# Kernel tuning notes

Measured on AMD Instinct MI355X. Metric: run time of the kernel, lower is better.

Reference implementation:

```python
import jax, jax.numpy as jnp
import numpy as np

B, L, D, N = 4, 2048, 1024, 8
H = D // N  # head_dim = 128
EPS = 1e-6


def _ln(x, gamma, beta, axes):
    m = jnp.mean(x, axis=axes, keepdims=True)
    v = jnp.mean(jnp.square(x - m), axis=axes, keepdims=True)
    return (x - m) * jax.lax.rsqrt(v + EPS) * gamma + beta


def setup_inputs() -> dict:
    key = jax.random.key(0)
    ks = jax.random.split(key, 8)
    glorot_d = (6.0 / (D + D)) ** 0.5  # GlorotUniform over fan_in=D, fan_out=N*H=D
    inputs = jax.random.normal(ks[0], (B, L, D), dtype=jnp.float32)
    attention_mask = jnp.tril(jnp.ones((L, L), dtype=bool))[None].repeat(B, axis=0)
    return {
        'inputs': inputs,
        'attention_mask': attention_mask,
        'ln_in_gamma': jnp.ones((D,), jnp.float32),
        'ln_in_beta': jnp.zeros((D,), jnp.float32),
        'wu': jax.random.uniform(ks[1], (D, N, H), jnp.float32, -glorot_d, glorot_d),
        'wq': jax.random.uniform(ks[2], (D, N, H), jnp.float32, -glorot_d, glorot_d),
        'wk': jax.random.uniform(ks[3], (D, N, H), jnp.float32, -glorot_d, glorot_d),
        'wv': jax.random.uniform(ks[4], (D, N, H), jnp.float32, -glorot_d, glorot_d),
        'ln_attn_gamma': jnp.ones((N, H), jnp.float32),
        'ln_attn_beta': jnp.zeros((N, H), jnp.float32),
        'wo': jax.random.uniform(ks[5], (N, H, D), jnp.float32, -glorot_d, glorot_d),
    }


def reference(inputs, attention_mask, ln_in_gamma, ln_in_beta, wu, wq, wk, wv,
              ln_attn_gamma, ln_attn_beta, wo):
    x = _ln(inputs, ln_in_gamma, ln_in_beta, axes=-1)  # [B,L,D]
    u = jax.nn.silu(jnp.einsum('btd,dnh->btnh', x, wu))
    q = jax.nn.silu(jnp.einsum('btd,dnh->btnh', x, wq))
    k = jax.nn.silu(jnp.einsum('btd,dnh->btnh', x, wk))
    v = jax.nn.silu(jnp.einsum('btd,dnh->btnh', x, wv))
    # pointwise silu attention, normalized by sequence length
    qk = jnp.einsum('bthd,bshd->bhts', q, k)  # [B,N,L,L]
    seq_len = q.shape[1]
    attn = jax.nn.silu(qk) / seq_len
    attn = jnp.where(attention_mask[:, None, :, :], attn, 0.0)
    attn_out = jnp.einsum('bhts,bshd->bthd', attn, v)  # [B,L,N,H]
    normed = _ln(attn_out, ln_attn_gamma, ln_attn_beta, axes=(-2, -1))
    out = jnp.einsum('btnh,nhd->btd', u * normed, wo)
    return out + inputs
```

## Files before the change

### kernel.cpp

```cpp
#include <hip/hip_runtime.h>
#include <hip/hip_bf16.h>
#include <stdint.h>

#define D_    1024
#define L_    2048
#define B_    4
#define NHEAD 8
#define HDIM  128
#define BL_   (B_*L_)
#define EPS_  1e-6f

typedef __attribute__((ext_vector_type(8))) short short8;
typedef __attribute__((ext_vector_type(4))) float f32x4;

__device__ __forceinline__ unsigned short f2bf(float f) {
  unsigned u = __builtin_bit_cast(unsigned, f);
  unsigned r = 0x7fffu + ((u >> 16) & 1u);
  return (unsigned short)((u + r) >> 16);
}
__device__ __forceinline__ float bf2f(unsigned short h) {
  return __builtin_bit_cast(float, ((unsigned)h) << 16);
}
__device__ __forceinline__ float silu_f(float x) {
  return x * __builtin_amdgcn_rcpf(1.f + __expf(-x));
}
__device__ __forceinline__ unsigned cvt_pk_bf16(float lo, float hi) {
  unsigned r;
  asm("v_cvt_pk_bf16_f32 %0, %1, %2" : "=v"(r) : "v"(lo), "v"(hi));
  return r;
}

__device__ __forceinline__ void gll16(const void* g, void* l) {
  auto gp = reinterpret_cast<const __attribute__((address_space(1))) unsigned*>(
      reinterpret_cast<uintptr_t>(g));
  auto lp = reinterpret_cast<__attribute__((address_space(3))) unsigned*>(
      (unsigned)reinterpret_cast<uintptr_t>(l));
  __builtin_amdgcn_global_load_lds(gp, lp, 16, 0, 0);
}

__global__ __launch_bounds__(256) void wt_kernel(
    const float* __restrict__ wu, const float* __restrict__ wq,
    const float* __restrict__ wk, const float* __restrict__ wv,
    const float* __restrict__ wo, unsigned short* __restrict__ wt)
{
  __shared__ float t[64][65];
  int mat = blockIdx.z;
  const float* src = mat==0?wu: mat==1?wq: mat==2?wk: mat==3?wv: wo;
  unsigned short* dst = wt + (size_t)mat*D_*D_;
  int r0 = blockIdx.y*64, c0 = blockIdx.x*64;
  int tid = threadIdx.x;
  for (int i = 0; i < 16; ++i) {
    int e = i*256 + tid; int r = e>>6, c = e&63;
    t[r][c] = src[(size_t)(r0+r)*D_ + c0 + c];
  }
  __syncthreads();
  for (int i = 0; i < 16; ++i) {
    int e = i*256 + tid; int r = e>>6, c = e&63;
    dst[(size_t)(c0+r)*D_ + r0 + c] = f2bf(t[c][r]);
  }
}

__global__ __launch_bounds__(256) void ln_in_kernel(
    const float* __restrict__ in, const float* __restrict__ gamma,
    const float* __restrict__ beta, unsigned short* __restrict__ x)
{
  int row = blockIdx.x, tid = threadIdx.x;
  float4 v = ((const float4*)(in + (size_t)row*D_))[tid];
  float s = v.x+v.y+v.z+v.w;
  float ss = v.x*v.x + v.y*v.y + v.z*v.z + v.w*v.w;
  #pragma unroll
  for (int o = 32; o; o >>= 1) { s += __shfl_down(s,o); ss += __shfl_down(ss,o); }
  __shared__ float red[8];
  int lane = tid&63, wid = tid>>6;
  if (lane==0) { red[wid]=s; red[4+wid]=ss; }
  __syncthreads();
  s = red[0]+red[1]+red[2]+red[3];
  ss = red[4]+red[5]+red[6]+red[7];
  float mean = s * (1.f/D_);
  float var  = ss * (1.f/D_) - mean*mean;
  float rstd = rsqrtf(var + EPS_);
  float4 g = ((const float4*)gamma)[tid], b = ((const float4*)beta)[tid];
  ushort4 o;
  o.x = f2bf((v.x-mean)*rstd*g.x + b.x);
  o.y = f2bf((v.y-mean)*rstd*g.y + b.y);
  o.z = f2bf((v.z-mean)*rstd*g.z + b.z);
  o.w = f2bf((v.w-mean)*rstd*g.w + b.w);
  ((ushort4*)(x + (size_t)row*D_))[tid] = o;
}

template<int MODE>
__global__ __launch_bounds__(512) __attribute__((amdgpu_waves_per_eu(2,2))) void gemm8p(
    const unsigned short* __restrict__ A, const unsigned short* __restrict__ Bt,
    unsigned short* __restrict__ o_u, unsigned short* __restrict__ o_q,
    unsigned short* __restrict__ o_k, unsigned short* __restrict__ o_vt,
    const float* __restrict__ resid, float* __restrict__ o_f)
{
  constexpr int BN  = (MODE==0) ? 256 : 128;
  constexpr int WN  = (MODE==0) ? 4 : 2;
  constexpr int WTM = (MODE==0) ? 128 : 64;
  constexpr int MF  = WTM/16;
  constexpr int BNS = BN*32;
  constexpr int BOFF = 32768;
  constexpr int RG  = BN/64;
  constexpr int NBCHW = (BNS/512)/8;
  const int K = 1024;

  __shared__ unsigned short lds[BOFF + 4*BNS];

  int lane = threadIdx.x & 63, wid = threadIdx.x >> 6;
  int wr = wid / WN, wc = wid % WN;
  int m0 = blockIdx.x * 256;
  int n0 = blockIdx.y * BN;
  const unsigned short* Ab = A + (size_t)m0*K;
  const unsigned short* Bb = Bt + (size_t)n0*K;

  f32x4 acc[MF][4] = {};

  auto stage = [&](int dbs, int k0) {
    #pragma unroll
    for (int j = 0; j < 2; ++j) {
      int c = wid*2 + j;
      int row = (c&3)*64 + lane;
      int kof = k0 + ((c>>2)<<3);
      gll16(Ab + (size_t)row*K + kof, &lds[dbs*8192 + c*512]);
    }
    #pragma unroll
    for (int j = 0; j < NBCHW; ++j) {
      int c = wid*NBCHW + j;
      int kk8 = c / RG, rg = c % RG;
      int row = rg*64 + lane;
      int kof = k0 + (kk8<<3);
      gll16(Bb + (size_t)row*K + kof, &lds[BOFF + dbs*BNS + c*512]);
    }
  };

  #pragma unroll
  for (int gp = 0; gp < 4; ++gp) stage(gp, gp*32);
  if constexpr (MODE==0) asm volatile("s_waitcnt vmcnt(12)" ::: "memory");
  else                   asm volatile("s_waitcnt vmcnt(9)"  ::: "memory");
  __builtin_amdgcn_s_barrier();

  auto do_phase = [&](int g, bool dostage) {
    const int bs = g & 3;
    const int kk4 = lane>>4, l15 = lane&15;
    short8 af[MF], bfr[4];
    const int ab = bs*8192 + kk4*2048 + (wr*WTM + l15)*8;
    #pragma unroll
    for (int m = 0; m < MF; ++m) af[m] = *(const short8*)&lds[ab + m*128];
    const int bb = BOFF + bs*BNS + kk4*(BN*8) + (wc*64 + l15)*8;
    #pragma unroll
    for (int n = 0; n < 4; ++n) bfr[n] = *(const short8*)&lds[bb + n*128];
    if (dostage) {
      int tp = g + 3;
      int k0 = (tp < 32 ? tp : 31) * 32;
      stage(tp & 3, k0);
    }
    __builtin_amdgcn_sched_barrier(0);
    __builtin_amdgcn_s_barrier();
    asm volatile("s_waitcnt lgkmcnt(0)" ::: "memory");
    __builtin_amdgcn_sched_barrier(0);
    __builtin_amdgcn_s_setprio(1);
    #pragma unroll
    for (int m = 0; m < MF; ++m)
      #pragma unroll
      for (int n = 0; n < 4; ++n)
        acc[m][n] = __builtin_amdgcn_mfma_f32_16x16x32_bf16(af[m], bfr[n], acc[m][n], 0,0,0);
    __builtin_amdgcn_s_setprio(0);
    if constexpr (MODE==0) asm volatile("s_waitcnt vmcnt(8)" ::: "memory");
    else                   asm volatile("s_waitcnt vmcnt(6)" ::: "memory");
    __builtin_amdgcn_sched_barrier(0);
    __builtin_amdgcn_s_barrier();
  };

  do_phase(0, false);
  #pragma unroll
  for (int g = 1; g < 32; ++g) do_phase(g, true);

  if constexpr (MODE == 0) {
    int mat = n0 >> 10;
    int jb = n0 & 1023;
    #pragma unroll
    for (int m = 0; m < MF; ++m) {
      int t_ = m0 + wr*WTM + m*16 + ((lane>>4)<<2);
      #pragma unroll
      for (int n = 0; n < 4; ++n) {
        int jj = jb + wc*64 + n*16 + (lane&15);
        float p0 = silu_f(acc[m][n][0]);
        float p1 = silu_f(acc[m][n][1]);
        float p2 = silu_f(acc[m][n][2]);
        float p3 = silu_f(acc[m][n][3]);
        if (mat == 3) {
          int b = t_ >> 11, tt = t_ & 2047;
          int nn = jj >> 7, h = jj & 127;
          ushort4 pk;
          pk.x = f2bf(p0); pk.y = f2bf(p1); pk.z = f2bf(p2); pk.w = f2bf(p3);
          *(ushort4*)&o_vt[(((size_t)(b*NHEAD+nn))*HDIM + h)*L_ + tt] = pk;
        } else {
          unsigned short* dst = mat==0 ? o_u : (mat==1 ? o_q : o_k);
          dst[(size_t)(t_+0)*D_ + jj] = f2bf(p0);
          dst[(size_t)(t_+1)*D_ + jj] = f2bf(p1);
          dst[(size_t)(t_+2)*D_ + jj] = f2bf(p2);
          dst[(size_t)(t_+3)*D_ + jj] = f2bf(p3);
        }
      }
    }
  } else {
    #pragma unroll
    for (int m = 0; m < MF; ++m) {
      int t_ = m0 + wr*WTM + m*16 + ((lane>>4)<<2);
      #pragma unroll
      for (int n = 0; n < 4; ++n) {
        int jj = n0 + wc*64 + n*16 + (lane&15);
        #pragma unroll
        for (int r = 0; r < 4; ++r)
          o_f[(size_t)(t_+r)*D_ + jj] = acc[m][n][r] + resid[(size_t)(t_+r)*D_ + jj];
      }
    }
  }
}

__global__ __launch_bounds__(512) __attribute__((amdgpu_waves_per_eu(2,2))) void attn_kernel(
    const unsigned short* __restrict__ gq, const unsigned short* __restrict__ gk,
    const unsigned short* __restrict__ gvt, unsigned short* __restrict__ attn_out)
{
  __shared__ unsigned short KP[16384];
  __shared__ unsigned short VT[16384];
  __shared__ unsigned short PA[16384];
  __shared__ unsigned short PB[16384];
  int id = blockIdx.x;
  int x = id & 7, c2 = (id >> 3) & 3, p = id >> 5;
  int bh = 8*c2 + x;
  int b = bh >> 3, n = bh & 7;
  int tiA = p, tiB = 15 - p;
  const unsigned short* qb = gq + (size_t)b*L_*D_ + n*HDIM;
  const unsigned short* kb = gk + (size_t)b*L_*D_ + n*HDIM;
  const unsigned short* vb = gvt + (size_t)bh*HDIM*L_;
  unsigned short* ob = attn_out + (size_t)b*L_*D_ + n*HDIM;
  int lane = threadIdx.x & 63, wid = threadIdx.x >> 6;
  int wsel = wid >> 2, wq = wid & 3;
  int wr = wq >> 1, wc = wq & 1;
  int hi = lane >> 4, l15 = lane & 15;
  int ti = wsel ? tiB : tiA;
  int t0 = ti * 128;
  unsigned short* Pbuf = wsel ? PB : PA;

  #pragma unroll
  for (int i = 0; i < 8; ++i) {
    int cc = wq*8 + i;
    int row = ((cc&1)<<6) + lane;
    int kof = (cc>>1)<<3;
    gll16(qb + (size_t)(t0+row)*D_ + kof, &Pbuf[cc*512]);
  }
  __syncthreads();
  short8 qf[4][4];
  #pragma unroll
  for (int kk = 0; kk < 4; ++kk) {
    int kbase = (kk*4 + hi)*1024;
    #pragma unroll
    for (int fn = 0; fn < 4; ++fn)
      qf[kk][fn] = *(const short8*)&Pbuf[kbase + (wc*64 + fn*16 + l15)*8];
  }
  __syncthreads();
  #pragma unroll
  for (int i = 0; i < 4; ++i) {
    int cc = wid*4 + i;
    int row = ((cc&1)<<6) + lane;
    int kof = (cc>>1)<<3;
    gll16(kb + (size_t)row*D_ + kof, &KP[cc*512]);
    gll16(vb + (size_t)row*L_ + kof, &VT[cc*512]);
  }
  __syncthreads();

  f32x4 oacc[4][4] = {};
  for (int st = 0; st <= tiB; ++st) {
    bool act = wsel ? true : (st <= tiA);
    bool stg = (st < tiB);
    f32x4 sacc[4][4] = {};
    if (act) {
      __builtin_amdgcn_s_setprio(1);
      #pragma unroll
      for (int kk = 0; kk < 4; ++kk) {
        int kbase = (kk*4 + hi)*1024;
        short8 kf[4];
        #pragma unroll
        for (int fm = 0; fm < 4; ++fm)
          kf[fm] = *(const short8*)&KP[kbase + (wr*64 + fm*16 + l15)*8];
        #pragma unroll
        for (int fm = 0; fm < 4; ++fm)
          #pragma unroll
          for (int fn = 0; fn < 4; ++fn)
            sacc[fm][fn] = __builtin_amdgcn_mfma_f32_16x16x32_bf16(kf[fm], qf[kk][fn], sacc[fm][fn], 0,0,0);
      }
      __builtin_amdgcn_s_setprio(0);
    }
    uint4 kreg[4];
    if (stg) {
      #pragma unroll
      for (int i = 0; i < 4; ++i) {
        int cc = wid*4 + i;
        int row = ((cc&1)<<6) + lane;
        int kof = (cc>>1)<<3;
        kreg[i] = *(const uint4*)(kb + (size_t)((st+1)*128 + row)*D_ + kof);
      }
    }
    if (act) {
      bool diag = (st == ti);
      #pragma unroll
      for (int fm = 0; fm < 4; ++fm) {
        int sb = wr*64 + fm*16 + (hi<<2);
        #pragma unroll
        for (int fn = 0; fn < 4; ++fn) {
          int tl = wc*64 + fn*16 + l15;
          float pv[4];
          #pragma unroll
          for (int r = 0; r < 4; ++r) {
            float sv = silu_f(sacc[fm][fn][r]) * (1.f/2048.f);
            if (diag && (tl < sb + r)) sv = 0.f;
            pv[r] = sv;
          }
          int a0 = (sb>>3)*1024 + tl*8 + (sb&7);
          *(unsigned*)&Pbuf[a0]   = cvt_pk_bf16(pv[0], pv[1]);
          *(unsigned*)&Pbuf[a0+2] = cvt_pk_bf16(pv[2], pv[3]);
        }
      }
    }
    asm volatile("s_waitcnt vmcnt(0) lgkmcnt(0)" ::: "memory");
    __builtin_amdgcn_sched_barrier(0);
    __builtin_amdgcn_s_barrier();
    __builtin_amdgcn_sched_barrier(0);
    if (stg) {
      #pragma unroll
      for (int i = 0; i < 4; ++i) {
        int cc = wid*4 + i;
        *(uint4*)&KP[cc*512 + (lane<<3)] = kreg[i];
      }
    }
    if (act) {
      __builtin_amdgcn_s_setprio(1);
      #pragma unroll
      for (int kk = 0; kk < 4; ++kk) {
        int kbase = (kk*4 + hi)*1024;
        short8 pa[4], vf[4];
        #pragma unroll
        for (int fm = 0; fm < 4; ++fm)
          pa[fm] = *(const short8*)&Pbuf[kbase + (wr*64 + fm*16 + l15)*8];
        #pragma unroll
        for (int fn = 0; fn < 4; ++fn)
          vf[fn] = *(const short8*)&VT[kbase + (wc*64 + fn*16 + l15)*8];
        #pragma unroll
        for (int fm = 0; fm < 4; ++fm)
          #pragma unroll
          for (int fn = 0; fn < 4; ++fn)
            oacc[fm][fn] = __builtin_amdgcn_mfma_f32_16x16x32_bf16(pa[fm], vf[fn], oacc[fm][fn], 0,0,0);
      }
      __builtin_amdgcn_s_setprio(0);
    }
    asm volatile("s_waitcnt lgkmcnt(0)" ::: "memory");
    __builtin_amdgcn_sched_barrier(0);
    __builtin_amdgcn_s_barrier();
    __builtin_amdgcn_sched_barrier(0);
    if (stg) {
      #pragma unroll
      for (int i = 0; i < 4; ++i) {
        int cc = wid*4 + i;
        int row = ((cc&1)<<6) + lane;
        int kof = (cc>>1)<<3;
        gll16(vb + (size_t)row*L_ + (st+1)*128 + kof, &VT[cc*512]);
      }
      __builtin_amdgcn_sched_barrier(0);
    }
  }
  #pragma unroll
  for (int fm = 0; fm < 4; ++fm) {
    int tl = wr*64 + fm*16 + (hi<<2);
    #pragma unroll
    for (int fn = 0; fn < 4; ++fn) {
      int h = wc*64 + fn*16 + l15;
      #pragma unroll
      for (int r = 0; r < 4; ++r)
        ob[(size_t)(t0 + tl + r)*D_ + h] = f2bf(oacc[fm][fn][r]);
    }
  }
}

__global__ __launch_bounds__(256) void ln_mul_kernel(
    const unsigned short* __restrict__ ain, const float* __restrict__ gamma,
    const float* __restrict__ beta, const unsigned short* __restrict__ u,
    unsigned short* __restrict__ y)
{
  int row = blockIdx.x, tid = threadIdx.x;
  ushort4 av = ((const ushort4*)(ain + (size_t)row*D_))[tid];
  float v0 = bf2f(av.x), v1 = bf2f(av.y), v2 = bf2f(av.z), v3 = bf2f(av.w);
  float s = v0+v1+v2+v3;
  float ss = v0*v0+v1*v1+v2*v2+v3*v3;
  #pragma unroll
  for (int o = 32; o; o >>= 1) { s += __shfl_down(s,o); ss += __shfl_down(ss,o); }
  __shared__ float red[8];
  int lane = tid&63, wid = tid>>6;
  if (lane==0) { red[wid]=s; red[4+wid]=ss; }
  __syncthreads();
  s = red[0]+red[1]+red[2]+red[3];
  ss = red[4]+red[5]+red[6]+red[7];
  float mean = s * (1.f/D_);
  float var  = ss * (1.f/D_) - mean*mean;
  float rstd = rsqrtf(var + EPS_);
  float4 g = ((const float4*)gamma)[tid], b = ((const float4*)beta)[tid];
  ushort4 uu = ((const ushort4*)(u + (size_t)row*D_))[tid];
  ushort4 o;
  o.x = f2bf(bf2f(uu.x) * ((v0-mean)*rstd*g.x + b.x));
  o.y = f2bf(bf2f(uu.y) * ((v1-mean)*rstd*g.y + b.y));
  o.z = f2bf(bf2f(uu.z) * ((v2-mean)*rstd*g.z + b.z));
  o.w = f2bf(bf2f(uu.w) * ((v3-mean)*rstd*g.w + b.w));
  ((ushort4*)(y + (size_t)row*D_))[tid] = o;
}

extern "C" void kernel_launch(void* const* d_in, const int* in_sizes, int n_in,
                              void* d_out, int out_size, void* d_ws, size_t ws_size,
                              hipStream_t stream) {
  const float* inputs = (const float*)d_in[0];
  const float* g_in = (const float*)d_in[2];
  const float* b_in = (const float*)d_in[3];
  const float* wu = (const float*)d_in[4];
  const float* wq = (const float*)d_in[5];
  const float* wk = (const float*)d_in[6];
  const float* wv = (const float*)d_in[7];
  const float* g_at = (const float*)d_in[8];
  const float* b_at = (const float*)d_in[9];
  const float* wo = (const float*)d_in[10];
  float* out = (float*)d_out;

  char* ws = (char*)d_ws;
  unsigned short* x   = (unsigned short*)(ws + ((size_t)0));
  unsigned short* q   = (unsigned short*)(ws + ((size_t)16<<20));
  unsigned short* k   = (unsigned short*)(ws + ((size_t)32<<20));
  unsigned short* u   = (unsigned short*)(ws + ((size_t)48<<20));
  unsigned short* vt  = (unsigned short*)(ws + ((size_t)64<<20));
  unsigned short* wt  = (unsigned short*)(ws + ((size_t)80<<20));
  unsigned short* ao  = (unsigned short*)(ws + ((size_t)96<<20));
  unsigned short* y = x;

  wt_kernel<<<dim3(16,16,5), 256, 0, stream>>>(wu, wq, wk, wv, wo, wt);
  ln_in_kernel<<<BL_, 256, 0, stream>>>(inputs, g_in, b_in, x);
  gemm8p<0><<<dim3(32,16), 512, 0, stream>>>(x, wt, u, q, k, vt, nullptr, nullptr);
  attn_kernel<<<256, 512, 0, stream>>>(q, k, vt, ao);
  ln_mul_kernel<<<BL_, 256, 0, stream>>>(ao, g_at, b_at, u, y);
  gemm8p<1><<<dim3(32,8), 512, 0, stream>>>(y, wt + (size_t)4*D_*D_,
                                            nullptr, nullptr, nullptr, nullptr, inputs, out);
}
```

Measured before the change: 279.9 us.

## Split attention KV range across wave groups and reduce partial outputs in LDS

Before, the two 4-wave groups of a block each handled a different query tile, paired p and 15-p, so the short-tile group sat idle for many steps. Now both groups work on the same query tile, and each takes half of every 128-key step (64 keys). The two query tiles are processed one after the other, and the partial outputs are summed through LDS before the store. This removes idle waves under the causal imbalance, at the cost of running both tiles in sequence, extra barriers, and an LDS reduction per tile.

New measurement: 257.0 us. 1.09x faster.

```diff
diff --git a/kernel.cpp b/kernel.cpp
--- a/kernel.cpp
+++ b/kernel.cpp
@@ -223,15 +223,11 @@
     const unsigned short* __restrict__ gq, const unsigned short* __restrict__ gk,
     const unsigned short* __restrict__ gvt, unsigned short* __restrict__ attn_out)
 {
-  __shared__ unsigned short KP[16384];
-  __shared__ unsigned short VT[16384];
-  __shared__ unsigned short PA[16384];
-  __shared__ unsigned short PB[16384];
+  __shared__ unsigned short SM[49152];
   int id = blockIdx.x;
-  int x = id & 7, c2 = (id >> 3) & 3, p = id >> 5;
+  int x = id & 7, c2 = (id >> 3) & 3, q = id >> 5;
   int bh = 8*c2 + x;
   int b = bh >> 3, n = bh & 7;
-  int tiA = p, tiB = 15 - p;
   const unsigned short* qb = gq + (size_t)b*L_*D_ + n*HDIM;
   const unsigned short* kb = gk + (size_t)b*L_*D_ + n*HDIM;
   const unsigned short* vb = gvt + (size_t)bh*HDIM*L_;
@@ -240,105 +236,102 @@
   int wsel = wid >> 2, wq = wid & 3;
   int wr = wq >> 1, wc = wq & 1;
   int hi = lane >> 4, l15 = lane & 15;
-  int ti = wsel ? tiB : tiA;
-  int t0 = ti * 128;
-  unsigned short* Pbuf = wsel ? PB : PA;
-
-  #pragma unroll
-  for (int i = 0; i < 8; ++i) {
-    int cc = wq*8 + i;
-    int row = ((cc&1)<<6) + lane;
-    int kof = (cc>>1)<<3;
-    gll16(qb + (size_t)(t0+row)*D_ + kof, &Pbuf[cc*512]);
-  }
-  __syncthreads();
-  short8 qf[4][4];
-  #pragma unroll
-  for (int kk = 0; kk < 4; ++kk) {
-    int kbase = (kk*4 + hi)*1024;
-    #pragma unroll
-    for (int fn = 0; fn < 4; ++fn)
-      qf[kk][fn] = *(const short8*)&Pbuf[kbase + (wc*64 + fn*16 + l15)*8];
-  }
-  __syncthreads();
-  #pragma unroll
-  for (int i = 0; i < 4; ++i) {
-    int cc = wid*4 + i;
-    int row = ((cc&1)<<6) + lane;
-    int kof = (cc>>1)<<3;
-    gll16(kb + (size_t)row*D_ + kof, &KP[cc*512]);
-    gll16(vb + (size_t)row*L_ + kof, &VT[cc*512]);
-  }
-  __syncthreads();
-
-  f32x4 oacc[4][4] = {};
-  for (int st = 0; st <= tiB; ++st) {
-    bool act = wsel ? true : (st <= tiA);
-    bool stg = (st < tiB);
-    f32x4 sacc[4][4] = {};
-    if (act) {
+  unsigned short* Kbuf = SM + (wsel ? 8192 : 0);
+  unsigned short* Vbuf = SM + 16384 + (wsel ? 8192 : 0);
+  unsigned short* Pbuf = SM + 32768 + (wsel ? 8192 : 0);
+  unsigned short* Qbuf = SM + 32768;
+  float* Cbuf = (float*)SM;
+
+  for (int uu = 0; uu < 2; ++uu) {
+    int ti = uu ? q : (15 - q);
+    int t0 = ti * 128;
+    #pragma unroll
+    for (int i = 0; i < 4; ++i) {
+      int cc = wid*4 + i;
+      gll16(qb + (size_t)(t0 + ((cc&1)<<6) + lane)*D_ + ((cc>>1)<<3), &Qbuf[cc*512]);
+    }
+    __syncthreads();
+    short8 qf[4][4];
+    #pragma unroll
+    for (int kk = 0; kk < 4; ++kk) {
+      int kbase = (kk*4 + hi)*1024;
+      #pragma unroll
+      for (int fn = 0; fn < 4; ++fn)
+        qf[kk][fn] = *(const short8*)&Qbuf[kbase + (wc*64 + fn*16 + l15)*8];
+    }
+    __syncthreads();
+    #pragma unroll
+    for (int i = 0; i < 4; ++i) {
+      int cc = wq*4 + i;
+      gll16(kb + (size_t)(wsel*64 + lane)*D_ + (cc<<3), &Kbuf[cc*512]);
+      gll16(vb + (size_t)(((cc&1)<<6) + lane)*L_ + wsel*64 + ((cc>>1)<<3), &Vbuf[cc*512]);
+    }
+    __syncthreads();
+
+    f32x4 oacc[4][4] = {};
+    for (int j = 0; j <= ti; ++j) {
+      bool stg = (j < ti);
+      int cnext = 2*(j+1) + wsel;
+      f32x4 sacc[2][4] = {};
       __builtin_amdgcn_s_setprio(1);
       #pragma unroll
       for (int kk = 0; kk < 4; ++kk) {
-        int kbase = (kk*4 + hi)*1024;
-        short8 kf[4];
-        #pragma unroll
-        for (int fm = 0; fm < 4; ++fm)
-          kf[fm] = *(const short8*)&KP[kbase + (wr*64 + fm*16 + l15)*8];
-        #pragma unroll
-        for (int fm = 0; fm < 4; ++fm)
+        int kbase = (kk*4 + hi)*512;
+        short8 kf[2];
+        #pragma unroll
+        for (int fm = 0; fm < 2; ++fm)
+          kf[fm] = *(const short8*)&Kbuf[kbase + (wr*32 + fm*16 + l15)*8];
+        #pragma unroll
+        for (int fm = 0; fm < 2; ++fm)
           #pragma unroll
           for (int fn = 0; fn < 4; ++fn)
             sacc[fm][fn] = __builtin_amdgcn_mfma_f32_16x16x32_bf16(kf[fm], qf[kk][fn], sacc[fm][fn], 0,0,0);
       }
       __builtin_amdgcn_s_setprio(0);
-    }
-    uint4 kreg[4];
-    if (stg) {
-      #pragma unroll
-      for (int i = 0; i < 4; ++i) {
-        int cc = wid*4 + i;
-        int row = ((cc&1)<<6) + lane;
-        int kof = (cc>>1)<<3;
-        kreg[i] = *(const uint4*)(kb + (size_t)((st+1)*128 + row)*D_ + kof);
-      }
-    }
-    if (act) {
-      bool diag = (st == ti);
-      #pragma unroll
-      for (int fm = 0; fm < 4; ++fm) {
-        int sb = wr*64 + fm*16 + (hi<<2);
-        #pragma unroll
-        for (int fn = 0; fn < 4; ++fn) {
-          int tl = wc*64 + fn*16 + l15;
-          float pv[4];
+      uint4 kreg[4];
+      if (stg) {
+        #pragma unroll
+        for (int i = 0; i < 4; ++i) {
+          int cc = wq*4 + i;
+          kreg[i] = *(const uint4*)(kb + (size_t)(cnext*64 + lane)*D_ + (cc<<3));
+        }
+      }
+      {
+        bool diag = (j == ti);
+        int maskoff = wsel*64;
+        #pragma unroll
+        for (int fm = 0; fm < 2; ++fm) {
+          int sb = wr*32 + fm*16 + (hi<<2);
           #pragma unroll
-          for (int r = 0; r < 4; ++r) {
-            float sv = silu_f(sacc[fm][fn][r]) * (1.f/2048.f);
-            if (diag && (tl < sb + r)) sv = 0.f;
-            pv[r] = sv;
+          for (int fn = 0; fn < 4; ++fn) {
+            int tl = wc*64 + fn*16 + l15;
+            float pv[4];
+            #pragma unroll
+            for (int r = 0; r < 4; ++r) {
+              float sv = silu_f(sacc[fm][fn][r]) * (1.f/2048.f);
+              if (diag && (tl < maskoff + sb + r)) sv = 0.f;
+              pv[r] = sv;
+            }
+            int a0 = (sb>>3)*1024 + tl*8 + (sb&7);
+            *(unsigned*)&Pbuf[a0]   = cvt_pk_bf16(pv[0], pv[1]);
+            *(unsigned*)&Pbuf[a0+2] = cvt_pk_bf16(pv[2], pv[3]);
           }
-          int a0 = (sb>>3)*1024 + tl*8 + (sb&7);
-          *(unsigned*)&Pbuf[a0]   = cvt_pk_bf16(pv[0], pv[1]);
-          *(unsigned*)&Pbuf[a0+2] = cvt_pk_bf16(pv[2], pv[3]);
-        }
-      }
-    }
-    asm volatile("s_waitcnt vmcnt(0) lgkmcnt(0)" ::: "memory");
-    __builtin_amdgcn_sched_barrier(0);
-    __builtin_amdgcn_s_barrier();
-    __builtin_amdgcn_sched_barrier(0);
-    if (stg) {
-      #pragma unroll
-      for (int i = 0; i < 4; ++i) {
-        int cc = wid*4 + i;
-        *(uint4*)&KP[cc*512 + (lane<<3)] = kreg[i];
-      }
-    }
-    if (act) {
+        }
+      }
+      asm volatile("s_waitcnt vmcnt(0) lgkmcnt(0)" ::: "memory");
+      __builtin_amdgcn_sched_barrier(0);
+      __builtin_amdgcn_s_barrier();
+      __builtin_amdgcn_sched_barrier(0);
+      if (stg) {
+        #pragma unroll
+        for (int i = 0; i < 4; ++i) {
+          int cc = wq*4 + i;
+          *(uint4*)&Kbuf[cc*512 + lane*8] = kreg[i];
+        }
+      }
       __builtin_amdgcn_s_setprio(1);
       #pragma unroll
-      for (int kk = 0; kk < 4; ++kk) {
+      for (int kk = 0; kk < 2; ++kk) {
         int kbase = (kk*4 + hi)*1024;
         short8 pa[4], vf[4];
         #pragma unroll
@@ -346,7 +339,7 @@
           pa[fm] = *(const short8*)&Pbuf[kbase + (wr*64 + fm*16 + l15)*8];
         #pragma unroll
         for (int fn = 0; fn < 4; ++fn)
-          vf[fn] = *(const short8*)&VT[kbase + (wc*64 + fn*16 + l15)*8];
+          vf[fn] = *(const short8*)&Vbuf[kbase + (wc*64 + fn*16 + l15)*8];
         #pragma unroll
         for (int fm = 0; fm < 4; ++fm)
           #pragma unroll
@@ -354,32 +347,51 @@
             oacc[fm][fn] = __builtin_amdgcn_mfma_f32_16x16x32_bf16(pa[fm], vf[fn], oacc[fm][fn], 0,0,0);
       }
       __builtin_amdgcn_s_setprio(0);
+      asm volatile("s_waitcnt lgkmcnt(0)" ::: "memory");
+      __builtin_amdgcn_sched_barrier(0);
+      __builtin_amdgcn_s_barrier();
+      __builtin_amdgcn_sched_barrier(0);
+      if (stg) {
+        #pragma unroll
+        for (int i = 0; i < 4; ++i) {
+          int cc = wq*4 + i;
+          gll16(vb + (size_t)(((cc&1)<<6) + lane)*L_ + cnext*64 + ((cc>>1)<<3), &Vbuf[cc*512]);
+        }
+        __builtin_amdgcn_sched_barrier(0);
+      }
+    }
+    if (wsel == 1) {
+      #pragma unroll
+      for (int fm = 0; fm < 4; ++fm) {
+        int tl = wr*64 + fm*16 + (hi<<2);
+        #pragma unroll
+        for (int fn = 0; fn < 4; ++fn) {
+          int h = wc*64 + fn*16 + l15;
+          #pragma unroll
+          for (int r = 0; r < 4; ++r)
+            Cbuf[(tl+r)*128 + h] = oacc[fm][fn][r];
+        }
+      }
     }
     asm volatile("s_waitcnt lgkmcnt(0)" ::: "memory");
-    __builtin_amdgcn_sched_barrier(0);
     __builtin_amdgcn_s_barrier();
     __builtin_amdgcn_sched_barrier(0);
-    if (stg) {
-      #pragma unroll
-      for (int i = 0; i < 4; ++i) {
-        int cc = wid*4 + i;
-        int row = ((cc&1)<<6) + lane;
-        int kof = (cc>>1)<<3;
-        gll16(vb + (size_t)row*L_ + (st+1)*128 + kof, &VT[cc*512]);
-      }
-      __builtin_amdgcn_sched_barrier(0);
-    }
-  }
-  #pragma unroll
-  for (int fm = 0; fm < 4; ++fm) {
-    int tl = wr*64 + fm*16 + (hi<<2);
-    #pragma unroll
-    for (int fn = 0; fn < 4; ++fn) {
-      int h = wc*64 + fn*16 + l15;
-      #pragma unroll
-      for (int r = 0; r < 4; ++r)
-        ob[(size_t)(t0 + tl + r)*D_ + h] = f2bf(oacc[fm][fn][r]);
-    }
+    if (wsel == 0) {
+      #pragma unroll
+      for (int fm = 0; fm < 4; ++fm) {
+        int tl = wr*64 + fm*16 + (hi<<2);
+        #pragma unroll
+        for (int fn = 0; fn < 4; ++fn) {
+          int h = wc*64 + fn*16 + l15;
+          #pragma unroll
+          for (int r = 0; r < 4; ++r) {
+            float v = oacc[fm][fn][r] + Cbuf[(tl+r)*128 + h];
+            ob[(size_t)(t0 + tl + r)*D_ + h] = f2bf(v);
+          }
+        }
+      }
+    }
+    __syncthreads();
   }
 }
 
```
